# Kernel tuning notes

Hardware: AMD Instinct MI355X
Metric: run time of the kernel (lower is better)

Reference implementation:

```python
import jax, jax.numpy as jnp
import numpy as np

N, E = 50000, 800000
IN_DIM, HID, OUT_DIM = 128, 96, 64
MAX_REC = 5


def setup_inputs() -> dict:
    key = jax.random.key(0)
    ks = jax.random.split(key, 10)
    g = lambda k, shape, scale: (jax.random.normal(k, shape, jnp.float32) * scale)
    return {
        "x": jax.random.normal(ks[0], (N, IN_DIM), jnp.float32),
        "edge_index": jax.random.randint(ks[1], (2, E), 0, N, jnp.int32),
        "w_in": g(ks[2], (IN_DIM, HID), 0.05),
        "b_in": jnp.zeros((HID,), jnp.float32),
        "tau_w1": g(ks[3], (IN_DIM, 16), 0.08),
        "tau_b1": jnp.zeros((16,), jnp.float32),
        "tau_w2": g(ks[4], (16, 1), 0.25),
        "tau_b2": jnp.zeros((1,), jnp.float32),
        "gru_wih": g(ks[5], (3 * HID, HID), 0.05),
        "gru_whh": g(ks[6], (3 * HID, HID), 0.05),
        "gru_bih": jnp.zeros((3 * HID,), jnp.float32),
        "gru_bhh": jnp.zeros((3 * HID,), jnp.float32),
        "w_out": g(ks[7], (HID, OUT_DIM), 0.05),
        "b_out": jnp.zeros((OUT_DIM,), jnp.float32),
    }


def _gru_cell(inp, h, wih, whh, bih, bhh):
    # torch.nn.GRUCell math; wih/whh are [3H, H] stacked (r, z, n)
    gi = inp @ wih.T + bih  # [N, 3H]
    gh = h @ whh.T + bhh    # [N, 3H]
    ir, iz, inn = jnp.split(gi, 3, axis=-1)
    hr, hz, hn = jnp.split(gh, 3, axis=-1)
    r = jax.nn.sigmoid(ir + hr)
    z = jax.nn.sigmoid(iz + hz)
    n = jnp.tanh(inn + r * hn)
    return (1.0 - z) * n + z * h


def reference(x, edge_index, w_in, b_in, tau_w1, tau_b1, tau_w2, tau_b2,
              gru_wih, gru_whh, gru_bih, gru_bhh, w_out, b_out):
    h = jax.nn.relu(x @ w_in + b_in)  # [N, H]
    tau_val = jax.nn.softplus(jax.nn.relu(x @ tau_w1 + tau_b1) @ tau_w2 + tau_b2)[:, 0]
    # .long() truncates toward zero; tau > 0 so trunc == floor via int cast
    steps = jnp.minimum((1.0 / tau_val).astype(jnp.int32), MAX_REC)  # [N]
    row, col = edge_index[0], edge_index[1]
    for _ in range(MAX_REC):
        d1 = jnp.abs(h[row] - h[col])                       # [E, H]
        agg = jax.ops.segment_sum(d1, row, num_segments=N)  # [N, H]
        new_h = _gru_cell(agg, h, gru_wih, gru_whh, gru_bih, gru_bhh)
        h = jnp.where((steps > 0)[:, None], new_h, h)
        steps = steps - 1
    return h @ w_out + b_out
```

## Files before the change

kernel.cpp:

```cpp
#include <hip/hip_runtime.h>
#include <hip/hip_bf16.h>

#define HID 96
#define INDIM 128
#define OUTDIM 64
#define BM 128
#define GP 128
#define NBF 512

typedef __attribute__((ext_vector_type(8))) _Float16 half8;
typedef __attribute__((ext_vector_type(4))) _Float16 half4;
typedef __attribute__((ext_vector_type(4))) float floatx4;
typedef __attribute__((ext_vector_type(4))) unsigned int uintx4;

__device__ __forceinline__ float ldmix(const void* p, long i, int mode) {
    return mode ? ((const float*)p)[i]
                : __bfloat162float(((const __hip_bfloat16*)p)[i]);
}

__global__ void sniff_kernel(const unsigned int* xw, int* mode) {
    int lane = threadIdx.x & 63;
    int cnt = 0;
    for (int i = lane; i < 4096; i += 64) {
        unsigned int low = xw[i] & 0xFFFFu;
        unsigned int e = (low >> 7) & 0xFFu;
        if (e >= 0xC0u) cnt++;
    }
    #pragma unroll
    for (int ofs = 32; ofs > 0; ofs >>= 1) cnt += __shfl_down(cnt, ofs);
    if (lane == 0) *mode = (cnt > 256) ? 1 : 0;
}

__global__ void prep_kernel(const void* w_in, const void* b_in, const void* tau_w1,
                            const void* tau_b1, const void* tau_w2, const void* tau_b2,
                            const void* wih, const void* whh, const void* bih, const void* bhh,
                            const void* w_out, const void* b_out,
                            _Float16* W2F, _Float16* WinF, _Float16* WoutF,
                            float* tau_w1_f, float* smallf, const int* mode) {
    int m = *mode;
    int tid = blockIdx.x*blockDim.x + threadIdx.x;
    if (tid < 384*192) {
        int c = tid / 192, k = tid % 192;
        int g = c / 96, jj = c % 96;
        float v = 0.f;
        if (k < 96) {
            if (g == 0)      v = ldmix(wih, (long)(jj)*96 + k, m);
            else if (g == 1) v = ldmix(wih, (long)(96+jj)*96 + k, m);
            else if (g == 2) v = ldmix(wih, (long)(192+jj)*96 + k, m);
        } else {
            int kk = k - 96;
            if (g == 0)      v = ldmix(whh, (long)(jj)*96 + kk, m);
            else if (g == 1) v = ldmix(whh, (long)(96+jj)*96 + kk, m);
            else if (g == 3) v = ldmix(whh, (long)(192+jj)*96 + kk, m);
        }
        W2F[tid] = (_Float16)v;
    }
    if (tid < 96*128) {
        int j = tid >> 7, k = tid & 127;
        WinF[tid] = (_Float16)ldmix(w_in, (long)k*96 + j, m);
    }
    if (tid < 64*96) {
        int j = tid / 96, k = tid % 96;
        WoutF[tid] = (_Float16)ldmix(w_out, (long)k*OUTDIM + j, m);
    }
    if (tid < INDIM*16)   tau_w1_f[tid] = ldmix(tau_w1, tid, m);
    if (tid < HID)    smallf[tid]       = ldmix(b_in, tid, m);
    if (tid < 3*HID){ smallf[96+tid]    = ldmix(bih, tid, m);
                      smallf[384+tid]   = ldmix(bhh, tid, m); }
    if (tid < OUTDIM) smallf[672+tid]   = ldmix(b_out, tid, m);
    if (tid < 16)   { smallf[736+tid]   = ldmix(tau_w2, tid, m);
                      smallf[752+tid]   = ldmix(tau_b1, tid, m); }
    if (tid == 0)     smallf[768]       = ldmix(tau_b2, 0, m);
}

__global__ void __launch_bounds__(512) h0_kernel(
        const void* __restrict__ x, const _Float16* __restrict__ WinF,
        const float* __restrict__ smallf, const int* __restrict__ mode,
        _Float16* __restrict__ hN, int N) {
    int row0 = blockIdx.x * BM;
    int jj0 = blockIdx.y * 16;

    __shared__ _Float16 Ah[128*136];
    __shared__ _Float16 Wh[16*136];

    int tid = threadIdx.x;
    int m = *mode;
    long limit = (long)N * INDIM;
    #pragma unroll
    for (int j = 0; j < 8; j++) {
        int e = (tid + j*512) * 4;
        int r = e >> 7, c = e & 127;
        long ge = (long)(row0 + r)*INDIM + c;
        half4 vh = {0, 0, 0, 0};
        if (ge + 4 <= limit) {
            if (m) {
                floatx4 v = *(const floatx4*)((const float*)x + ge);
                #pragma unroll
                for (int q = 0; q < 4; q++) vh[q] = (_Float16)v[q];
            } else {
                const __hip_bfloat16* p = (const __hip_bfloat16*)x + ge;
                #pragma unroll
                for (int q = 0; q < 4; q++) vh[q] = (_Float16)__bfloat162float(p[q]);
            }
        }
        *(half4*)(&Ah[r*136 + c]) = vh;
    }
    if (tid < 256) {
        int wrow = tid >> 4;
        int k = (tid & 15) * 8;
        *(half8*)(&Wh[wrow*136 + k]) = *(const half8*)(WinF + (long)(jj0 + wrow)*INDIM + k);
    }
    __syncthreads();

    int lane = tid & 63;
    int w = tid >> 6;
    int m15 = lane & 15, quad = lane >> 4;
    floatx4 acc = {0.f, 0.f, 0.f, 0.f};
    int abase = (w*16 + m15)*136 + quad*8;
    #pragma unroll
    for (int ks = 0; ks < 4; ks++) {
        int k0 = ks*32;
        half8 a = *(const half8*)(&Ah[abase + k0]);
        half8 b = *(const half8*)(&Wh[m15*136 + quad*8 + k0]);
        acc = __builtin_amdgcn_mfma_f32_16x16x32_f16(a, b, acc, 0, 0, 0);
    }

    int jj = jj0 + m15;
    float b = smallf[jj];
    #pragma unroll
    for (int reg = 0; reg < 4; reg++) {
        int li = row0 + w*16 + quad*4 + reg;
        if (li < N) hN[(long)li*HID + jj] = (_Float16)fmaxf(acc[reg] + b, 0.f);
    }
}

__global__ void __launch_bounds__(256) tau_kernel(
        const void* __restrict__ x, const float* __restrict__ tw,
        const float* __restrict__ smallf, const int* __restrict__ mode,
        int* __restrict__ steps, int N) {
    int n = blockIdx.x*blockDim.x + threadIdx.x;
    int m = *mode;
    int nc = (n < N) ? n : (N - 1);

    float xr[128];
    if (m) {
        const floatx4* xp = (const floatx4*)x + (size_t)nc*32;
        #pragma unroll
        for (int ks = 0; ks < 32; ks++) {
            floatx4 v = xp[ks];
            xr[ks*4+0] = v[0]; xr[ks*4+1] = v[1];
            xr[ks*4+2] = v[2]; xr[ks*4+3] = v[3];
        }
    } else {
        const uintx4* xp = (const uintx4*)((const __hip_bfloat16*)x + (size_t)nc*128);
        #pragma unroll
        for (int ks = 0; ks < 16; ks++) {
            uintx4 v = xp[ks];
            #pragma unroll
            for (int q = 0; q < 4; q++) {
                unsigned int w = v[q];
                xr[ks*8 + q*2 + 0] = __uint_as_float((w & 0xFFFFu) << 16);
                xr[ks*8 + q*2 + 1] = __uint_as_float(w & 0xFFFF0000u);
            }
        }
    }

    float acc[16];
    #pragma unroll
    for (int j = 0; j < 16; j++) acc[j] = 0.f;
    #pragma unroll
    for (int k = 0; k < 128; k++) {
        float xv = xr[k];
        #pragma unroll
        for (int j = 0; j < 16; j++) acc[j] += xv * tw[k*16 + j];
    }

    float z = smallf[768];
    #pragma unroll
    for (int j = 0; j < 16; j++)
        z += fmaxf(acc[j] + smallf[752 + j], 0.f) * smallf[736 + j];
    float tau = fmaxf(z, 0.f) + log1pf(expf(-fabsf(z)));
    float inv = 1.0f / tau;
    int s;
    if (inv >= 5.0f) s = 5;
    else { s = (int)inv; if (s < 0) s = 0; if (s > 5) s = 5; }
    if (n < N) steps[n] = s;
}

__global__ void __launch_bounds__(512) bincnt_kernel(
        const int* __restrict__ row, int E, int NB, int shift, int* __restrict__ bincnt) {
    __shared__ int h[NBF];
    int tid = threadIdx.x;
    int bs = blockDim.x;
    for (int i = tid; i < NB; i += bs) h[i] = 0;
    __syncthreads();
    int stride = gridDim.x * bs;
    for (int e = blockIdx.x*bs + tid; e < E; e += stride)
        atomicAdd(&h[row[e] >> shift], 1);
    __syncthreads();
    for (int i = tid; i < NB; i += bs) {
        int c = h[i];
        if (c) atomicAdd(&bincnt[i], c);
    }
}

__global__ void binscan_kernel(const int* __restrict__ bincnt, int NB, int E, int N,
                               int* __restrict__ bin_start, int* __restrict__ bincur,
                               int* __restrict__ off) {
    __shared__ int vals[NBF];
    __shared__ int part[256];
    int tid = threadIdx.x;
    int per = (NB + 255) / 256;
    int base = tid * per;
    int s = 0;
    for (int j = 0; j < per; j++) {
        int i = base + j;
        int v = (i < NB) ? bincnt[i] : 0;
        if (i < NBF) vals[i] = s;
        s += v;
    }
    part[tid] = s;
    __syncthreads();
    for (int ofs = 1; ofs < 256; ofs <<= 1) {
        int t = (tid >= ofs) ? part[tid - ofs] : 0;
        __syncthreads();
        part[tid] += t;
        __syncthreads();
    }
    int add = (tid == 0) ? 0 : part[tid - 1];
    for (int j = 0; j < per; j++) {
        int i = base + j;
        if (i < NB) {
            int v = vals[i] + add;
            bin_start[i] = v;
            bincur[i] = v;
        }
    }
    if (tid == 0) { bin_start[NB] = E; off[N] = E; }
}

__global__ void __launch_bounds__(512) binfill_kernel(
        const int* __restrict__ row, const int* __restrict__ col,
        int E, int NB, int shift, int* __restrict__ bincur,
        unsigned int* __restrict__ binbuf) {
    __shared__ int h[NBF];
    __shared__ int bs[NBF];
    int tid = threadIdx.x;
    int bsz = blockDim.x;
    int chunk = (E + gridDim.x - 1) / gridDim.x;
    int c0 = blockIdx.x * chunk;
    int c1 = min(c0 + chunk, E);
    for (int i = tid; i < NB; i += bsz) h[i] = 0;
    __syncthreads();
    for (int e = c0 + tid; e < c1; e += bsz)
        atomicAdd(&h[row[e] >> shift], 1);
    __syncthreads();
    for (int i = tid; i < NB; i += bsz) {
        int c = h[i];
        if (c) { bs[i] = atomicAdd(&bincur[i], c); h[i] = 0; }
    }
    __syncthreads();
    unsigned int mask = (1u << shift) - 1u;
    for (int e = c0 + tid; e < c1; e += bsz) {
        int r = row[e];
        int b = r >> shift;
        int p = atomicAdd(&h[b], 1);
        binbuf[bs[b] + p] = ((unsigned int)(r & mask) << 24) | (unsigned int)col[e];
    }
}

__global__ void __launch_bounds__(256) bincsr_kernel(
        const unsigned int* __restrict__ binbuf,
        const int* __restrict__ bin_start, int N, int shift,
        int* __restrict__ off, int* __restrict__ csr_col) {
    __shared__ int hist[256];
    __shared__ int pfx[256];
    int b = blockIdx.x;
    int tid = threadIdx.x;
    int BINSZ = 1 << shift;
    int s0 = bin_start[b], s1 = bin_start[b + 1];
    if (tid < BINSZ) hist[tid] = 0;
    __syncthreads();
    for (int e = s0 + tid; e < s1; e += 256)
        atomicAdd(&hist[binbuf[e] >> 24], 1);
    __syncthreads();
    if (tid == 0) {
        int run = 0;
        for (int j = 0; j < BINSZ; j++) { pfx[j] = run; run += hist[j]; }
    }
    __syncthreads();
    if (tid < BINSZ) {
        int node = (b << shift) + tid;
        if (node < N) off[node] = s0 + pfx[tid];
        hist[tid] = pfx[tid];
    }
    __syncthreads();
    for (int e = s0 + tid; e < s1; e += 256) {
        unsigned int pk = binbuf[e];
        int lr = pk >> 24;
        int p = atomicAdd(&hist[lr], 1);
        csr_col[s0 + p] = (int)(pk & 0xFFFFFFu);
    }
}

__global__ void partial_kernel(const int* __restrict__ steps, int N, int C,
                               int* __restrict__ blksum) {
    __shared__ int red[256*8];
    int tid = threadIdx.x;
    int tg = blockIdx.x*256 + tid;
    int start = tg*C, end = min(start + C, N);
    if (end < start) end = start;
    int cnt[6] = {0,0,0,0,0,0};
    for (int i = start; i < end; i++) cnt[steps[i]]++;
    #pragma unroll
    for (int k = 0; k < 6; k++) red[tid*8 + k] = cnt[k];
    __syncthreads();
    for (int ofs = 128; ofs > 0; ofs >>= 1) {
        if (tid < ofs) {
            #pragma unroll
            for (int k = 0; k < 6; k++) red[tid*8 + k] += red[(tid+ofs)*8 + k];
        }
        __syncthreads();
    }
    if (tid < 6) blksum[blockIdx.x*8 + tid] = red[tid];
}

__global__ void base_kernel(const int* __restrict__ blksum, int* __restrict__ bstart,
                            int* __restrict__ blkbase) {
    __shared__ int tot[8];
    __shared__ int sb[8];
    int tid = threadIdx.x;
    if (tid < 6) {
        int s = 0;
        for (int b = 0; b < GP; b++) s += blksum[b*8 + tid];
        tot[tid] = s;
    }
    __syncthreads();
    if (tid == 0) {
        int run = 0;
        for (int ss = 5; ss >= 0; --ss) { sb[ss] = run; bstart[ss] = run; run += tot[ss]; }
        bstart[6] = run;
    }
    __syncthreads();
    if (tid < 6) {
        int run = sb[tid];
        for (int b = 0; b < GP; b++) { blkbase[b*8 + tid] = run; run += blksum[b*8 + tid]; }
    }
}

__global__ void scatter_kernel(const int* __restrict__ steps, const int* __restrict__ blkbase,
                               int N, int C, int* __restrict__ order) {
    __shared__ int buf[256];
    int tid = threadIdx.x;
    int b = blockIdx.x;
    int tg = b*256 + tid;
    int start = tg*C, end = min(start + C, N);
    if (end < start) end = start;
    int cnt[6] = {0,0,0,0,0,0};
    for (int i = start; i < end; i++) cnt[steps[i]]++;
    int mybase[6];
    #pragma unroll
    for (int k = 0; k < 6; k++) {
        buf[tid] = cnt[k];
        __syncthreads();
        for (int ofs = 1; ofs < 256; ofs <<= 1) {
            int t = (tid >= ofs) ? buf[tid - ofs] : 0;
            __syncthreads();
            buf[tid] += t;
            __syncthreads();
        }
        mybase[k] = blkbase[b*8 + k] + buf[tid] - cnt[k];
        __syncthreads();
    }
    for (int i = start; i < end; i++) order[mybase[steps[i]]++] = i;
}

__global__ void pack_kernel(const _Float16* __restrict__ hN, const int* __restrict__ order,
                            _Float16* __restrict__ hF, int N) {
    int tid = blockIdx.x*blockDim.x + threadIdx.x;
    if (tid >= N*HID) return;
    int li = tid / HID, f = tid % HID;
    int n = order[li];
    hF[tid] = hN[(size_t)n*HID + f];
}

__global__ void agg_kernel(const _Float16* __restrict__ hN, const int* __restrict__ off,
                           const int* __restrict__ csr_col, const int* __restrict__ order,
                           const int* __restrict__ bstart, int t, _Float16* __restrict__ aggF) {
    int K = bstart[t];
    int total = K * 12;
    int stride = gridDim.x * blockDim.x;
    for (int idx = blockIdx.x*blockDim.x + threadIdx.x; idx < total; idx += stride) {
        int li = idx / 12, fg = idx % 12;
        int f = fg * 8;
        int i = order[li];
        half8 hv = *(const half8*)(hN + (size_t)i*HID + f);
        float hvf[8];
        #pragma unroll
        for (int q = 0; q < 8; q++) hvf[q] = (float)hv[q];
        int e0 = off[i], e1 = off[i+1];
        float acc[8];
        #pragma unroll
        for (int q = 0; q < 8; q++) acc[q] = 0.f;
        int e = e0;
        for (; e + 4 <= e1; e += 4) {
            int c0 = csr_col[e],   c1 = csr_col[e+1];
            int c2 = csr_col[e+2], c3 = csr_col[e+3];
            half8 v0 = *(const half8*)(hN + (size_t)c0*HID + f);
            half8 v1 = *(const half8*)(hN + (size_t)c1*HID + f);
            half8 v2 = *(const half8*)(hN + (size_t)c2*HID + f);
            half8 v3 = *(const half8*)(hN + (size_t)c3*HID + f);
            #pragma unroll
            for (int q = 0; q < 8; q++) {
                acc[q] += fabsf(hvf[q] - (float)v0[q]) + fabsf(hvf[q] - (float)v1[q])
                        + fabsf(hvf[q] - (float)v2[q]) + fabsf(hvf[q] - (float)v3[q]);
            }
        }
        for (; e < e1; e++) {
            int c = csr_col[e];
            half8 v = *(const half8*)(hN + (size_t)c*HID + f);
            #pragma unroll
            for (int q = 0; q < 8; q++) acc[q] += fabsf(hvf[q] - (float)v[q]);
        }
        half8 outv;
        #pragma unroll
        for (int q = 0; q < 8; q++) outv[q] = (_Float16)acc[q];
        *(half8*)(aggF + (size_t)li*HID + f) = outv;
    }
}

__global__ void __launch_bounds__(512) gru_kernel(
        const _Float16* __restrict__ aggF, const _Float16* __restrict__ hFin,
        const _Float16* __restrict__ W2F,
        const float* __restrict__ smallf, const int* __restrict__ bstart, int t,
        const int* __restrict__ order, _Float16* __restrict__ hN,
        _Float16* __restrict__ hFout, int N) {
    int K = bstart[t];
    int row0 = blockIdx.x * BM;
    if (row0 >= K) return;
    int jj0 = blockIdx.y * 16;

    __shared__ _Float16 Ah[128*200];
    __shared__ _Float16 Wh[64*200];

    int tid = threadIdx.x;
    long limit = (long)N * HID;
    #pragma unroll
    for (int j = 0; j < 3; j++) {
        int e = (tid + j*512) * 8;
        {
            int r = e / 96, c = e % 96;
            long ge = (long)(row0 + r)*96 + c;
            half8 va = {0,0,0,0,0,0,0,0}, vh = va;
            if (ge + 8 <= limit) {
                va = *(const half8*)(aggF + ge);
                vh = *(const half8*)(hFin + ge);
            }
            *(half8*)(&Ah[r*200 + c])      = va;
            *(half8*)(&Ah[r*200 + 96 + c]) = vh;
        }
        {
            int wrow = e / 192, k = e % 192;
            int g = wrow >> 4, cc = wrow & 15;
            *(half8*)(&Wh[wrow*200 + k]) = *(const half8*)(W2F + (long)(g*96 + jj0 + cc)*192 + k);
        }
    }
    __syncthreads();

    int lane = tid & 63;
    int w = tid >> 6;
    int m15 = lane & 15, quad = lane >> 4;
    floatx4 acc[4];
    #pragma unroll
    for (int g = 0; g < 4; g++) acc[g] = (floatx4){0.f, 0.f, 0.f, 0.f};

    int abase = (w*16 + m15)*200 + quad*8;
    #pragma unroll
    for (int ks = 0; ks < 6; ks++) {
        int k0 = ks*32;
        half8 a = *(const half8*)(&Ah[abase + k0]);
        #pragma unroll
        for (int g = 0; g < 4; g++) {
            half8 b = *(const half8*)(&Wh[(g*16 + m15)*200 + quad*8 + k0]);
            acc[g] = __builtin_amdgcn_mfma_f32_16x16x32_f16(a, b, acc[g], 0, 0, 0);
        }
    }

    int jj = jj0 + m15;
    float bir = smallf[96+jj],  biz = smallf[192+jj], bin = smallf[288+jj];
    float bhr = smallf[384+jj], bhz = smallf[480+jj], bhn = smallf[576+jj];
    #pragma unroll
    for (int reg = 0; reg < 4; reg++) {
        int li = row0 + w*16 + quad*4 + reg;
        if (li < K) {
            float rp = acc[0][reg] + bir + bhr;
            float zp = acc[1][reg] + biz + bhz;
            float ip = acc[2][reg] + bin;
            float hn = acc[3][reg] + bhn;
            float r  = 1.f/(1.f + expf(-rp));
            float z  = 1.f/(1.f + expf(-zp));
            float nn = tanhf(ip + r*hn);
            int tr = w*16 + quad*4 + reg;
            float hold = (float)Ah[tr*200 + 96 + jj];
            _Float16 v16 = (_Float16)((1.f - z)*nn + z*hold);
            int node = order[li];
            hN[(long)node*HID + jj] = v16;
            hFout[(long)li*HID + jj] = v16;
        }
    }
}

__global__ void __launch_bounds__(512) out_kernel(
        const _Float16* __restrict__ hN, const _Float16* __restrict__ WoutF,
        const float* __restrict__ smallf, void* out, const int* mode, int N) {
    int row0 = blockIdx.x * BM;
    int jj0 = blockIdx.y * 16;

    __shared__ _Float16 Ah[128*104];
    __shared__ _Float16 Wh[16*104];

    int tid = threadIdx.x;
    long limit = (long)N * HID;
    #pragma unroll
    for (int j = 0; j < 3; j++) {
        int e = (tid + j*512) * 8;
        int r = e / 96, c = e % 96;
        long ge = (long)(row0 + r)*HID + c;
        half8 v = {0,0,0,0,0,0,0,0};
        if (ge + 8 <= limit) v = *(const half8*)(hN + ge);
        *(half8*)(&Ah[r*104 + c]) = v;
    }
    if (tid < 192) {
        int wrow = tid / 12;
        int k = (tid % 12) * 8;
        *(half8*)(&Wh[wrow*104 + k]) = *(const half8*)(WoutF + (long)(jj0 + wrow)*HID + k);
    }
    __syncthreads();

    int lane = tid & 63;
    int w = tid >> 6;
    int m15 = lane & 15, quad = lane >> 4;
    floatx4 acc = {0.f, 0.f, 0.f, 0.f};
    int abase = (w*16 + m15)*104 + quad*8;
    #pragma unroll
    for (int ks = 0; ks < 3; ks++) {
        int k0 = ks*32;
        half8 a = *(const half8*)(&Ah[abase + k0]);
        half8 b = *(const half8*)(&Wh[m15*104 + quad*8 + k0]);
        acc = __builtin_amdgcn_mfma_f32_16x16x32_f16(a, b, acc, 0, 0, 0);
    }

    int jj = jj0 + m15;
    float b = smallf[672+jj];
    int m = *mode;
    #pragma unroll
    for (int reg = 0; reg < 4; reg++) {
        int li = row0 + w*16 + quad*4 + reg;
        if (li < N) {
            float v = acc[reg] + b;
            long oi = (long)li*OUTDIM + jj;
            if (m) ((float*)out)[oi] = v;
            else   ((__hip_bfloat16*)out)[oi] = __float2bfloat16(v);
        }
    }
}

extern "C" void kernel_launch(void* const* d_in, const int* in_sizes, int n_in,
                              void* d_out, int out_size, void* d_ws, size_t ws_size,
                              hipStream_t stream) {
    const void* x      = d_in[0];
    const int*  ei     = (const int*)d_in[1];
    const void* w_in   = d_in[2],  *b_in   = d_in[3];
    const void* tau_w1 = d_in[4],  *tau_b1 = d_in[5];
    const void* tau_w2 = d_in[6],  *tau_b2 = d_in[7];
    const void* wih    = d_in[8],  *whh    = d_in[9];
    const void* bih    = d_in[10], *bhh    = d_in[11];
    const void* w_out  = d_in[12], *b_out  = d_in[13];

    int N = in_sizes[0] / INDIM;
    int E = in_sizes[1] / 2;
    const int* row = ei;
    const int* col = ei + E;

    int shift = 7;
    while ((((N + (1 << shift) - 1) >> shift)) > NBF && shift < 8) shift++;
    int NB = (N + (1 << shift) - 1) >> shift;

    char* ws = (char*)d_ws;
    size_t o = 0;
    auto take = [&](size_t bytes) -> char* {
        char* p = ws + o;
        o = (o + bytes + 255) & ~(size_t)255;
        return p;
    };
    _Float16* hN    = (_Float16*)take((size_t)N*HID*2);
    _Float16* hFa   = (_Float16*)take((size_t)N*HID*2);
    _Float16* hFb   = (_Float16*)take((size_t)N*HID*2);
    _Float16* aggF  = (_Float16*)take((size_t)N*HID*2);
    _Float16* W2F   = (_Float16*)take((size_t)384*192*2);
    _Float16* WinF  = (_Float16*)take((size_t)96*128*2);
    _Float16* WoutF = (_Float16*)take((size_t)64*96*2);
    float* tau_w1_f = (float*)take((size_t)INDIM*16*4);
    float* smallf   = (float*)take(1024*4);
    int*   off      = (int*)take((size_t)(N+1)*4);
    int*   csr_col  = (int*)take((size_t)E*4);
    int*   order    = (int*)take((size_t)N*4);
    int*   steps    = (int*)take((size_t)N*4);
    int*   bstart   = (int*)take(64);
    int*   mode     = (int*)take(64);
    int*   blksum   = (int*)take((size_t)GP*8*4);
    int*   blkbase  = (int*)take((size_t)GP*8*4);
    unsigned int* binbuf = (unsigned int*)take((size_t)E*4);
    int*   bin_start = (int*)take((size_t)(NBF+1)*4);
    int*   bincur    = (int*)take((size_t)NBF*4);
    char*  zbase    = ws + o;
    int*   bincnt   = (int*)take((size_t)NBF*4);
    size_t zbytes   = (size_t)((ws + o) - zbase);

    hipMemsetAsync(zbase, 0, zbytes, stream);
    sniff_kernel<<<1, 64, 0, stream>>>((const unsigned int*)x, mode);

    prep_kernel<<<(384*192 + 255)/256, 256, 0, stream>>>(
        w_in, b_in, tau_w1, tau_b1, tau_w2, tau_b2, wih, whh, bih, bhh, w_out, b_out,
        W2F, WinF, WoutF, tau_w1_f, smallf, mode);

    dim3 hgrid((N + BM - 1)/BM, 6);
    h0_kernel<<<hgrid, 512, 0, stream>>>(x, WinF, smallf, mode, hN, N);
    tau_kernel<<<(N + 255)/256, 256, 0, stream>>>(x, tau_w1_f, smallf, mode, steps, N);

    bincnt_kernel<<<256, 512, 0, stream>>>(row, E, NB, shift, bincnt);
    binscan_kernel<<<1, 256, 0, stream>>>(bincnt, NB, E, N, bin_start, bincur, off);
    binfill_kernel<<<256, 512, 0, stream>>>(row, col, E, NB, shift, bincur, binbuf);
    bincsr_kernel<<<NB, 256, 0, stream>>>(binbuf, bin_start, N, shift, off, csr_col);

    int C = (N + GP*256 - 1) / (GP*256);
    partial_kernel<<<GP, 256, 0, stream>>>(steps, N, C, blksum);
    base_kernel<<<1, 64, 0, stream>>>(blksum, bstart, blkbase);
    scatter_kernel<<<GP, 256, 0, stream>>>(steps, blkbase, N, C, order);

    pack_kernel<<<(N*HID + 255)/256, 256, 0, stream>>>(hN, order, hFa, N);

    dim3 ggrid((N + BM - 1)/BM, 6);
    _Float16* hin = hFa;
    _Float16* hout = hFb;
    for (int t = 0; t < 5; t++) {
        agg_kernel<<<4096, 256, 0, stream>>>(hN, off, csr_col, order, bstart, t, aggF);
        gru_kernel<<<ggrid, 512, 0, stream>>>(aggF, hin, W2F, smallf, bstart, t,
                                              order, hN, hout, N);
        _Float16* tmp = hin; hin = hout; hout = tmp;
    }

    dim3 ogrid((N + BM - 1)/BM, 4);
    out_kernel<<<ogrid, 512, 0, stream>>>(hN, WoutF, smallf, d_out, mode, N);
}
```

Before: 348.6 us.

## Cache fp16 input in tau kernel, widen pack copies, triple agg per-thread work

The tau kernel now also writes an fp16 copy of x, and h0 reads that compact copy instead of reconverting fp32/bf16 x six times across its grid columns. The pack kernel copies 8 halves per thread instead of one. The aggregation kernel handles three 8-feature groups per thread, so each edge's column index and offset are loaded once per node instead of three times. The changes add an extra x-sized write, raise register pressure in the aggregation kernel, and cut the number of threads available to hide gather latency.

Measured after the change: 592.5 us. 1.7x slower.

```diff
diff --git a/kernel.cpp b/kernel.cpp
--- a/kernel.cpp
+++ b/kernel.cpp
@@ -73,71 +73,10 @@
     if (tid == 0)     smallf[768]       = ldmix(tau_b2, 0, m);
 }
 
-__global__ void __launch_bounds__(512) h0_kernel(
-        const void* __restrict__ x, const _Float16* __restrict__ WinF,
-        const float* __restrict__ smallf, const int* __restrict__ mode,
-        _Float16* __restrict__ hN, int N) {
-    int row0 = blockIdx.x * BM;
-    int jj0 = blockIdx.y * 16;
-
-    __shared__ _Float16 Ah[128*136];
-    __shared__ _Float16 Wh[16*136];
-
-    int tid = threadIdx.x;
-    int m = *mode;
-    long limit = (long)N * INDIM;
-    #pragma unroll
-    for (int j = 0; j < 8; j++) {
-        int e = (tid + j*512) * 4;
-        int r = e >> 7, c = e & 127;
-        long ge = (long)(row0 + r)*INDIM + c;
-        half4 vh = {0, 0, 0, 0};
-        if (ge + 4 <= limit) {
-            if (m) {
-                floatx4 v = *(const floatx4*)((const float*)x + ge);
-                #pragma unroll
-                for (int q = 0; q < 4; q++) vh[q] = (_Float16)v[q];
-            } else {
-                const __hip_bfloat16* p = (const __hip_bfloat16*)x + ge;
-                #pragma unroll
-                for (int q = 0; q < 4; q++) vh[q] = (_Float16)__bfloat162float(p[q]);
-            }
-        }
-        *(half4*)(&Ah[r*136 + c]) = vh;
-    }
-    if (tid < 256) {
-        int wrow = tid >> 4;
-        int k = (tid & 15) * 8;
-        *(half8*)(&Wh[wrow*136 + k]) = *(const half8*)(WinF + (long)(jj0 + wrow)*INDIM + k);
-    }
-    __syncthreads();
-
-    int lane = tid & 63;
-    int w = tid >> 6;
-    int m15 = lane & 15, quad = lane >> 4;
-    floatx4 acc = {0.f, 0.f, 0.f, 0.f};
-    int abase = (w*16 + m15)*136 + quad*8;
-    #pragma unroll
-    for (int ks = 0; ks < 4; ks++) {
-        int k0 = ks*32;
-        half8 a = *(const half8*)(&Ah[abase + k0]);
-        half8 b = *(const half8*)(&Wh[m15*136 + quad*8 + k0]);
-        acc = __builtin_amdgcn_mfma_f32_16x16x32_f16(a, b, acc, 0, 0, 0);
-    }
-
-    int jj = jj0 + m15;
-    float b = smallf[jj];
-    #pragma unroll
-    for (int reg = 0; reg < 4; reg++) {
-        int li = row0 + w*16 + quad*4 + reg;
-        if (li < N) hN[(long)li*HID + jj] = (_Float16)fmaxf(acc[reg] + b, 0.f);
-    }
-}
-
 __global__ void __launch_bounds__(256) tau_kernel(
         const void* __restrict__ x, const float* __restrict__ tw,
         const float* __restrict__ smallf, const int* __restrict__ mode,
-        int* __restrict__ steps, int N) {
+        int* __restrict__ steps, _Float16* __restrict__ xF, int N) {
     int n = blockIdx.x*blockDim.x + threadIdx.x;
     int m = *mode;
     int nc = (n < N) ? n : (N - 1);
@@ -165,6 +104,16 @@
         }
     }
 
+    if (n < N) {
+        #pragma unroll
+        for (int ks = 0; ks < 16; ks++) {
+            half8 vh;
+            #pragma unroll
+            for (int q = 0; q < 8; q++) vh[q] = (_Float16)xr[ks*8 + q];
+            *(half8*)(xF + (size_t)n*INDIM + ks*8) = vh;
+        }
+    }
+
     float acc[16];
     #pragma unroll
     for (int j = 0; j < 16; j++) acc[j] = 0.f;
@@ -187,6 +136,55 @@
     if (n < N) steps[n] = s;
 }
 
+__global__ void __launch_bounds__(512) h0_kernel(
+        const _Float16* __restrict__ xF, const _Float16* __restrict__ WinF,
+        const float* __restrict__ smallf, _Float16* __restrict__ hN, int N) {
+    int row0 = blockIdx.x * BM;
+    int jj0 = blockIdx.y * 16;
+
+    __shared__ _Float16 Ah[128*136];
+    __shared__ _Float16 Wh[16*136];
+
+    int tid = threadIdx.x;
+    long limit = (long)N * INDIM;
+    #pragma unroll
+    for (int j = 0; j < 4; j++) {
+        int e = (tid + j*512) * 8;
+        int r = e >> 7, c = e & 127;
+        long ge = (long)(row0 + r)*INDIM + c;
+        half8 vh = {0,0,0,0,0,0,0,0};
+        if (ge + 8 <= limit) vh = *(const half8*)(xF + ge);
+        *(half8*)(&Ah[r*136 + c]) = vh;
+    }
+    if (tid < 256) {
+        int wrow = tid >> 4;
+        int k = (tid & 15) * 8;
+        *(half8*)(&Wh[wrow*136 + k]) = *(const half8*)(WinF + (long)(jj0 + wrow)*INDIM + k);
+    }
+    __syncthreads();
+
+    int lane = tid & 63;
+    int w = tid >> 6;
+    int m15 = lane & 15, quad = lane >> 4;
+    floatx4 acc = {0.f, 0.f, 0.f, 0.f};
+    int abase = (w*16 + m15)*136 + quad*8;
+    #pragma unroll
+    for (int ks = 0; ks < 4; ks++) {
+        int k0 = ks*32;
+        half8 a = *(const half8*)(&Ah[abase + k0]);
+        half8 b = *(const half8*)(&Wh[m15*136 + quad*8 + k0]);
+        acc = __builtin_amdgcn_mfma_f32_16x16x32_f16(a, b, acc, 0, 0, 0);
+    }
+
+    int jj = jj0 + m15;
+    float b = smallf[jj];
+    #pragma unroll
+    for (int reg = 0; reg < 4; reg++) {
+        int li = row0 + w*16 + quad*4 + reg;
+        if (li < N) hN[(long)li*HID + jj] = (_Float16)fmaxf(acc[reg] + b, 0.f);
+    }
+}
+
 __global__ void __launch_bounds__(512) bincnt_kernel(
         const int* __restrict__ row, int E, int NB, int shift, int* __restrict__ bincnt) {
     __shared__ int h[NBF];
@@ -378,54 +376,75 @@
 __global__ void pack_kernel(const _Float16* __restrict__ hN, const int* __restrict__ order,
                             _Float16* __restrict__ hF, int N) {
     int tid = blockIdx.x*blockDim.x + threadIdx.x;
-    if (tid >= N*HID) return;
-    int li = tid / HID, f = tid % HID;
+    if (tid >= N*12) return;
+    int li = tid / 12, fg = tid % 12;
     int n = order[li];
-    hF[tid] = hN[(size_t)n*HID + f];
+    *(half8*)(hF + (size_t)li*HID + fg*8) = *(const half8*)(hN + (size_t)n*HID + fg*8);
 }
 
 __global__ void agg_kernel(const _Float16* __restrict__ hN, const int* __restrict__ off,
                            const int* __restrict__ csr_col, const int* __restrict__ order,
                            const int* __restrict__ bstart, int t, _Float16* __restrict__ aggF) {
     int K = bstart[t];
-    int total = K * 12;
+    int total = K * 4;
     int stride = gridDim.x * blockDim.x;
     for (int idx = blockIdx.x*blockDim.x + threadIdx.x; idx < total; idx += stride) {
-        int li = idx / 12, fg = idx % 12;
+        int li = idx >> 2, fg = idx & 3;
         int f = fg * 8;
         int i = order[li];
-        half8 hv = *(const half8*)(hN + (size_t)i*HID + f);
-        float hvf[8];
-        #pragma unroll
-        for (int q = 0; q < 8; q++) hvf[q] = (float)hv[q];
+        const _Float16* hb = hN + (size_t)i*HID + f;
+        half8 g0 = *(const half8*)(hb);
+        half8 g1 = *(const half8*)(hb + 32);
+        half8 g2 = *(const half8*)(hb + 64);
+        float hv0[8], hv1[8], hv2[8];
+        #pragma unroll
+        for (int q = 0; q < 8; q++) { hv0[q] = (float)g0[q]; hv1[q] = (float)g1[q]; hv2[q] = (float)g2[q]; }
+        float a0[8], a1[8], a2[8];
+        #pragma unroll
+        for (int q = 0; q < 8; q++) { a0[q] = 0.f; a1[q] = 0.f; a2[q] = 0.f; }
         int e0 = off[i], e1 = off[i+1];
-        float acc[8];
-        #pragma unroll
-        for (int q = 0; q < 8; q++) acc[q] = 0.f;
         int e = e0;
         for (; e + 4 <= e1; e += 4) {
             int c0 = csr_col[e],   c1 = csr_col[e+1];
             int c2 = csr_col[e+2], c3 = csr_col[e+3];
-            half8 v0 = *(const half8*)(hN + (size_t)c0*HID + f);
-            half8 v1 = *(const half8*)(hN + (size_t)c1*HID + f);
-            half8 v2 = *(const half8*)(hN + (size_t)c2*HID + f);
-            half8 v3 = *(const half8*)(hN + (size_t)c3*HID + f);
+            const _Float16* p0 = hN + (size_t)c0*HID + f;
+            const _Float16* p1 = hN + (size_t)c1*HID + f;
+            const _Float16* p2 = hN + (size_t)c2*HID + f;
+            const _Float16* p3 = hN + (size_t)c3*HID + f;
+            half8 v00 = *(const half8*)(p0),      v01 = *(const half8*)(p0 + 32), v02 = *(const half8*)(p0 + 64);
+            half8 v10 = *(const half8*)(p1),      v11 = *(const half8*)(p1 + 32), v12 = *(const half8*)(p1 + 64);
+            half8 v20 = *(const half8*)(p2),      v21 = *(const half8*)(p2 + 32), v22 = *(const half8*)(p2 + 64);
+            half8 v30 = *(const half8*)(p3),      v31 = *(const half8*)(p3 + 32), v32 = *(const half8*)(p3 + 64);
             #pragma unroll
             for (int q = 0; q < 8; q++) {
-                acc[q] += fabsf(hvf[q] - (float)v0[q]) + fabsf(hvf[q] - (float)v1[q])
-                        + fabsf(hvf[q] - (float)v2[q]) + fabsf(hvf[q] - (float)v3[q]);
+                a0[q] += fabsf(hv0[q] - (float)v00[q]) + fabsf(hv0[q] - (float)v10[q])
+                       + fabsf(hv0[q] - (float)v20[q]) + fabsf(hv0[q] - (float)v30[q]);
+                a1[q] += fabsf(hv1[q] - (float)v01[q]) + fabsf(hv1[q] - (float)v11[q])
+                       + fabsf(hv1[q] - (float)v21[q]) + fabsf(hv1[q] - (float)v31[q]);
+                a2[q] += fabsf(hv2[q] - (float)v02[q]) + fabsf(hv2[q] - (float)v12[q])
+                       + fabsf(hv2[q] - (float)v22[q]) + fabsf(hv2[q] - (float)v32[q]);
             }
         }
         for (; e < e1; e++) {
             int c = csr_col[e];
-            half8 v = *(const half8*)(hN + (size_t)c*HID + f);
+            const _Float16* p = hN + (size_t)c*HID + f;
+            half8 v0 = *(const half8*)(p);
+            half8 v1 = *(const half8*)(p + 32);
+            half8 v2 = *(const half8*)(p + 64);
             #pragma unroll
-            for (int q = 0; q < 8; q++) acc[q] += fabsf(hvf[q] - (float)v[q]);
-        }
-        half8 outv;
-        #pragma unroll
-        for (int q = 0; q < 8; q++) outv[q] = (_Float16)acc[q];
-        *(half8*)(aggF + (size_t)li*HID + f) = outv;
+            for (int q = 0; q < 8; q++) {
+                a0[q] += fabsf(hv0[q] - (float)v0[q]);
+                a1[q] += fabsf(hv1[q] - (float)v1[q]);
+                a2[q] += fabsf(hv2[q] - (float)v2[q]);
+            }
+        }
+        half8 o0, o1, o2;
+        #pragma unroll
+        for (int q = 0; q < 8; q++) { o0[q] = (_Float16)a0[q]; o1[q] = (_Float16)a1[q]; o2[q] = (_Float16)a2[q]; }
+        _Float16* ob = aggF + (size_t)li*HID + f;
+        *(half8*)(ob)      = o0;
+        *(half8*)(ob + 32) = o1;
+        *(half8*)(ob + 64) = o2;
     }
 }
 
@@ -597,6 +616,7 @@
     _Float16* hFa   = (_Float16*)take((size_t)N*HID*2);
     _Float16* hFb   = (_Float16*)take((size_t)N*HID*2);
     _Float16* aggF  = (_Float16*)take((size_t)N*HID*2);
+    _Float16* xF    = (_Float16*)take((size_t)N*INDIM*2);
     _Float16* W2F   = (_Float16*)take((size_t)384*192*2);
     _Float16* WinF  = (_Float16*)take((size_t)96*128*2);
     _Float16* WoutF = (_Float16*)take((size_t)64*96*2);
@@ -624,9 +644,10 @@
         w_in, b_in, tau_w1, tau_b1, tau_w2, tau_b2, wih, whh, bih, bhh, w_out, b_out,
         W2F, WinF, WoutF, tau_w1_f, smallf, mode);
 
+    tau_kernel<<<(N + 255)/256, 256, 0, stream>>>(x, tau_w1_f, smallf, mode, steps, xF, N);
+
     dim3 hgrid((N + BM - 1)/BM, 6);
-    h0_kernel<<<hgrid, 512, 0, stream>>>(x, WinF, smallf, mode, hN, N);
-    tau_kernel<<<(N + 255)/256, 256, 0, stream>>>(x, tau_w1_f, smallf, mode, steps, N);
+    h0_kernel<<<hgrid, 512, 0, stream>>>(xF, WinF, smallf, hN, N);
 
     bincnt_kernel<<<256, 512, 0, stream>>>(row, E, NB, shift, bincnt);
     binscan_kernel<<<1, 256, 0, stream>>>(bincnt, NB, E, N, bin_start, bincur, off);
@@ -638,7 +659,7 @@
     base_kernel<<<1, 64, 0, stream>>>(blksum, bstart, blkbase);
     scatter_kernel<<<GP, 256, 0, stream>>>(steps, blkbase, N, C, order);
 
-    pack_kernel<<<(N*HID + 255)/256, 256, 0, stream>>>(hN, order, hFa, N);
+    pack_kernel<<<(N*12 + 255)/256, 256, 0, stream>>>(hN, order, hFa, N);
 
     dim3 ggrid((N + BM - 1)/BM, 6);
     _Float16* hin = hFa;
```
